# Optimization experiments

Measured on AMD Instinct MI355X. Metric: run time of the kernel, lower is better.

The kernel has to match this reference:

```python
import jax, jax.numpy as jnp
import numpy as np

D = 256   # model dim
M = 64    # num mechanisms
B = 4
S = 8192


def setup_inputs() -> dict:
    key = jax.random.key(0)
    ks = jax.random.split(key, 16)
    n = jax.random.normal
    inp = {
        "x": n(ks[0], (B, S, D), jnp.float32),
        "context": n(ks[1], (B, S, D), jnp.float32),
        # stacked per-mechanism params (m, out, in) etc.
        "Wm": n(ks[2], (M, D, D), jnp.float32) * (1.0 / np.sqrt(D)),
        "bm": n(ks[3], (M, D), jnp.float32) * 0.02,
        "cm": n(ks[4], (M, D), jnp.float32),           # characteristics (1,1,dim) per node
        "um": n(ks[5], (M, D), jnp.float32) * (1.0 / np.sqrt(D)),  # timing_gate weight
        "vm": n(ks[6], (M,), jnp.float32) * 0.02,       # timing_gate bias
        # selector: Linear(d, 2d) -> GELU -> Linear(2d, m)
        "W1": n(ks[7], (2 * D, D), jnp.float32) * (1.0 / np.sqrt(D)),
        "b1": n(ks[8], (2 * D,), jnp.float32) * 0.02,
        "W2": n(ks[9], (M, 2 * D), jnp.float32) * (1.0 / np.sqrt(2 * D)),
        "b2": n(ks[10], (M,), jnp.float32) * 0.02,
        # integrate: Linear(2d, d)
        "Wi": n(ks[11], (D, 2 * D), jnp.float32) * (1.0 / np.sqrt(2 * D)),
        "bi": n(ks[12], (D,), jnp.float32) * 0.02,
    }
    return inp


def reference(x, context, Wm, bm, cm, um, vm, W1, b1, W2, b2, Wi, bi):
    # selector: softmax over mechanisms (b, s, m)
    h = jax.nn.gelu(jnp.einsum('bsd,ed->bse', context, W1) + b1, approximate=False)
    scores = jax.nn.softmax(jnp.einsum('bse,me->bsm', h, W2) + b2, axis=-1)

    # per-mechanism sigmoid timing gate (b, s, m)
    gate = jax.nn.sigmoid(jnp.einsum('bsd,md->bsm', x, um) + vm)

    # combined weight a[b,s,m] = softmax_score * gate; then
    # selected = sum_m a * (x @ Wm.T + bm + cm)  -- contracted without
    # materializing the (b, s, m, d) stack the torch loop builds.
    a = scores * gate                               # (b, s, m)
    selected = jnp.einsum('bsm,bse,mde->bsd', a, x, Wm) \
             + jnp.einsum('bsm,md->bsd', a, bm + cm)

    # integrate(concat([x, selected]))
    cat = jnp.concatenate([x, selected], axis=-1)   # (b, s, 2d)
    integrated = jnp.einsum('bse,de->bsd', cat, Wi) + bi
    return integrated
```

## Files before the change

kernel.cpp:

```cpp
#include <hip/hip_runtime.h>
#include <cstdint>
#include <cstddef>


typedef _Float16 f16;
typedef f16 f16x8 __attribute__((ext_vector_type(8)));
typedef float f32x4 __attribute__((ext_vector_type(4)));
typedef float f32x16 __attribute__((ext_vector_type(16)));

#define DEV __device__ __forceinline__

DEV uint32_t swz128(uint32_t b) { return b ^ (((b >> 7) & 7u) << 4); }

DEV void gload_lds16(const void* g, void* l) {
  __builtin_amdgcn_global_load_lds(
      (const __attribute__((address_space(1))) unsigned int*)g,
      (__attribute__((address_space(3))) unsigned int*)l, 16, 0, 0);
}

DEV f16x8 cvt8(float4 u0, float4 u1) {
  f16x8 v = {(f16)u0.x, (f16)u0.y, (f16)u0.z, (f16)u0.w,
             (f16)u1.x, (f16)u1.y, (f16)u1.z, (f16)u1.w};
  return v;
}

__global__ void prep_b_kernel(const float* __restrict__ S, f16* __restrict__ dst,
                              int K, int BN, int total) {
  int t = blockIdx.x * 256 + threadIdx.x;
  if (t >= total) return;
  int gpc = BN * 8;
  int g = t % gpc;
  int c = (t / gpc) % (K / 64);
  int cb = t / (gpc * (K / 64));
  int ks = g / (BN * 4);
  int rem = g % (BN * 4);
  int col = rem >> 2;
  int kg = rem & 3;
  int J = cb * BN + col;
  int k = c * 64 + ks * 32 + kg * 8;
  const float* s = S + (size_t)J * K + k;
  float4 u0 = *(const float4*)s;
  float4 u1 = *(const float4*)(s + 4);
  f16* chunk = dst + (size_t)(cb * (K / 64) + c) * (BN * 64);
  *(f16x8*)((char*)chunk + swz128((uint32_t)g * 16)) = cvt8(u0, u1);
}

__global__ void prep_wcat_kernel(const float* __restrict__ Wm,
                                 const float* __restrict__ bm,
                                 const float* __restrict__ cm,
                                 f16* __restrict__ dst) {
  int t = blockIdx.x * 256 + threadIdx.x;
  if (t >= 4 * 257 * 512) return;
  int g = t & 511;
  int gc = t >> 9;
  int c = gc % 257;
  int cb = gc / 257;
  int kstep = g >> 7;
  int khalf = (g >> 6) & 1;
  int col = cb * 64 + (g & 63);
  int k0 = kstep * 16 + khalf * 8;
  f16x8 v;
  if (c < 256) {
    int m = c & 63;
    int e0 = (c >> 6) * 64 + k0;
    const float* s = Wm + ((size_t)m * 256 + col) * 256 + e0;
    float4 u0 = *(const float4*)s;
    float4 u1 = *(const float4*)(s + 4);
    v = cvt8(u0, u1);
  } else {
#pragma unroll
    for (int j = 0; j < 8; ++j) {
      int k = k0 + j;
      v[j] = (f16)(bm[k * 256 + col] + cm[k * 256 + col]);
    }
  }
  *(f16x8*)(dst + ((size_t)(cb * 260 + c)) * 4096 + (size_t)g * 8) = v;
}

template <int BN, int NCHUNK, int A0C, int EPI>
__global__ __launch_bounds__(BN == 256 ? 512 : 256, 2)
void gemm_tpl(const float* __restrict__ A0, int lda0,
              const f16* __restrict__ A1, int lda1,
              const f16* __restrict__ Bt,
              const float* __restrict__ bias,
              float* __restrict__ outF, f16* __restrict__ outH, int ldo) {
  constexpr int WAVES = (BN == 256) ? 8 : 4;
  constexpr int THREADS = WAVES * 64;
  constexpr int WC = (BN == 256) ? 4 : 1;
  constexpr int WR = WAVES / WC;
  constexpr int RT = 128 / (WR * 16);
  constexpr int CT = (BN / WC) / 16;

  __shared__ alignas(16) f16 sA[2][128 * 64];
  __shared__ alignas(16) f16 sB[2][BN * 64];

  const int tid = threadIdx.x;
  const int lane = tid & 63;
  const int wid = tid >> 6;
  const int wr = wid / WC, wc = wid % WC;
  const int rb = blockIdx.x, cb = blockIdx.y;

  auto stageB = [&](int c, int buf) {
    const char* src = (const char*)(Bt + (size_t)(cb * NCHUNK + c) * (BN * 64));
#pragma unroll
    for (int it = 0; it < (BN * 64 * 2) / (THREADS * 16); ++it) {
      int off = (it * THREADS + tid) * 16;
      gload_lds16(src + off, (char*)&sB[buf][0] + off);
    }
  };
  auto stageA = [&](int c, int buf) {
#pragma unroll
    for (int it = 0; it < 1024 / THREADS; ++it) {
      int gg = it * THREADS + tid;
      int row = gg >> 3, eg = gg & 7;
      size_t rowG = (size_t)rb * 128 + row;
      f16x8 v;
      if (A0C > 0 && c < A0C) {
        const float* s = A0 + rowG * lda0 + c * 64 + eg * 8;
        float4 u0 = *(const float4*)s;
        float4 u1 = *(const float4*)(s + 4);
        v = cvt8(u0, u1);
      } else {
        v = *(const f16x8*)(A1 + rowG * lda1 + (c - A0C) * 64 + eg * 8);
      }
      *(f16x8*)((char*)&sA[buf][0] + swz128((uint32_t)(row * 128 + eg * 16))) = v;
    }
  };

  f32x4 acc[RT][CT];
#pragma unroll
  for (int i = 0; i < RT; ++i)
#pragma unroll
    for (int j = 0; j < CT; ++j) acc[i][j] = (f32x4){0.f, 0.f, 0.f, 0.f};

  stageB(0, 0);
  stageA(0, 0);
  __syncthreads();

  for (int c = 0; c < NCHUNK; ++c) {
    int cur = c & 1;
    if (c + 1 < NCHUNK) {
      stageB(c + 1, cur ^ 1);
      stageA(c + 1, cur ^ 1);
    }
#pragma unroll
    for (int ks = 0; ks < 2; ++ks) {
      f16x8 af[RT], bf[CT];
#pragma unroll
      for (int rt = 0; rt < RT; ++rt) {
        int row = wr * (RT * 16) + rt * 16 + (lane & 15);
        af[rt] = *(const f16x8*)((const char*)&sA[cur][0] +
                                 swz128((uint32_t)(row * 128 + ks * 64 + (lane >> 4) * 16)));
      }
#pragma unroll
      for (int ct = 0; ct < CT; ++ct) {
        int col = wc * (CT * 16) + ct * 16 + (lane & 15);
        bf[ct] = *(const f16x8*)((const char*)&sB[cur][0] +
                                 swz128((uint32_t)(((ks * BN + col) * 4 + (lane >> 4)) * 16)));
      }
#pragma unroll
      for (int rt = 0; rt < RT; ++rt)
#pragma unroll
        for (int ct = 0; ct < CT; ++ct)
          acc[rt][ct] = __builtin_amdgcn_mfma_f32_16x16x32_f16(af[rt], bf[ct], acc[rt][ct], 0, 0, 0);
    }
    __syncthreads();
  }

#pragma unroll
  for (int rt = 0; rt < RT; ++rt)
#pragma unroll
    for (int ct = 0; ct < CT; ++ct)
#pragma unroll
      for (int i = 0; i < 4; ++i) {
        size_t row = (size_t)rb * 128 + wr * (RT * 16) + rt * 16 + (lane >> 4) * 4 + i;
        int colG = cb * BN + wc * (CT * 16) + ct * 16 + (lane & 15);
        float v = acc[rt][ct][i];
        if constexpr (EPI == 0) {
          if (bias) v += bias[colG];
          outF[row * ldo + colG] = v;
        } else {
          v += bias[colG];
          float ge = 0.5f * v * (1.0f + erff(v * 0.70710678118f));
          outH[row * ldo + colG] = (f16)ge;
        }
      }
}

__global__ void selector_finish(const float* __restrict__ logits,
                                const float* __restrict__ glog,
                                const float* __restrict__ b2,
                                const float* __restrict__ vm,
                                f16* __restrict__ a16s) {
  int n = blockIdx.x * 4 + (threadIdx.x >> 6);
  int m = threadIdx.x & 63;
  float l = logits[(size_t)n * 64 + m] + b2[m];
  float mx = l;
#pragma unroll
  for (int o = 32; o; o >>= 1) mx = fmaxf(mx, __shfl_xor(mx, o));
  float p = expf(l - mx);
  float s = p;
#pragma unroll
  for (int o = 32; o; o >>= 1) s += __shfl_xor(s, o);
  float g = glog[(size_t)n * 64 + m] + vm[m];
  float gate = 1.0f / (1.0f + expf(-g));
  int rb = n >> 8, row = n & 255, gg = m >> 3, j = m & 7;
  a16s[(size_t)rb * 16384 + gg * 2048 + row * 8 + j] = (f16)(p / s * gate);
}

__global__ __launch_bounds__(256, 2)
void big_gemm(const float* __restrict__ x, const f16* __restrict__ a16s,
              const f16* __restrict__ Wcat, f16* __restrict__ sel) {
  __shared__ alignas(16) f16 sAa[8 * 256 * 8];

  const int tid = threadIdx.x;
  const int lane = tid & 63;
  const int wid = tid >> 6;
  const int l31 = lane & 31;
  const int khalf = lane >> 5;
  const int bid = blockIdx.x;
  const int xcd = bid & 7;
  const int cb = xcd >> 1;
  const int rb = (xcd & 1) * 64 + (bid >> 3);
  const char* Wb = (const char*)(Wcat + (size_t)cb * 260 * 4096);
  const int rbase = wid * 64 + l31;

  {
    const char* aSrc = (const char*)(a16s + (size_t)rb * 16384);
#pragma unroll
    for (int it = 0; it < 8; ++it) {
      int off = (it * 256 + tid) * 16;
      gload_lds16(aSrc + off, (char*)sAa + off);
    }
  }
  asm volatile("s_waitcnt vmcnt(0)" ::: "memory");
  __builtin_amdgcn_s_barrier();

  const int bOff = khalf * 1024 + l31 * 16;

  f32x16 acc[2][2];
#pragma unroll
  for (int i = 0; i < 2; ++i)
#pragma unroll
    for (int j = 0; j < 2; ++j)
#pragma unroll
      for (int r = 0; r < 16; ++r) acc[i][j][r] = 0.f;

  f16x8 xv[2][4];
  auto loadXV = [&](int er) {
#pragma unroll
    for (int rt = 0; rt < 2; ++rt)
#pragma unroll
      for (int ks = 0; ks < 4; ++ks) {
        const float* s = x + ((size_t)rb * 256 + rbase + rt * 32) * 256
                           + er * 64 + ks * 16 + khalf * 8;
        float4 u0 = *(const float4*)s;
        float4 u1 = *(const float4*)(s + 4);
        xv[rt][ks] = cvt8(u0, u1);
      }
  };
  loadXV(0);

  f16x8 bf0[8], bf1[8];
#pragma unroll
  for (int ks = 0; ks < 4; ++ks)
#pragma unroll
    for (int ct = 0; ct < 2; ++ct) {
      bf0[ks * 2 + ct] = *(const f16x8*)(Wb + 0 * 8192 + bOff + ks * 2048 + ct * 512);
      bf1[ks * 2 + ct] = *(const f16x8*)(Wb + 1 * 8192 + bOff + ks * 2048 + ct * 512);
    }

  for (int q8g = 0; q8g < 32; ++q8g) {
    const int q8 = q8g * 8;
    if ((q8 & 63) == 0 && q8 > 0) loadXV(q8 >> 6);
    f16x8 as_cur[2];
    {
      int g = (q8 & 63) >> 3;
#pragma unroll
      for (int rt = 0; rt < 2; ++rt)
        as_cur[rt] = *(const f16x8*)((const char*)sAa + ((g * 256) + rbase + rt * 32) * 16);
    }
#pragma unroll
    for (int u = 0; u < 8; ++u) {
      const int q = q8 + u;
      f16x8 af[2][4];
#pragma unroll
      for (int rt = 0; rt < 2; ++rt)
#pragma unroll
        for (int ks = 0; ks < 4; ++ks)
          af[rt][ks] = xv[rt][ks] * as_cur[rt][u];
      const char* nsrc = Wb + (size_t)(q + 2) * 8192 + bOff;
      if ((u & 1) == 0) {
        __builtin_amdgcn_s_setprio(1);
#pragma unroll
        for (int ks = 0; ks < 4; ++ks)
#pragma unroll
          for (int rt = 0; rt < 2; ++rt)
#pragma unroll
            for (int ct = 0; ct < 2; ++ct)
              acc[rt][ct] = __builtin_amdgcn_mfma_f32_32x32x16_f16(
                  af[rt][ks], bf0[ks * 2 + ct], acc[rt][ct], 0, 0, 0);
        __builtin_amdgcn_s_setprio(0);
#pragma unroll
        for (int ks = 0; ks < 4; ++ks)
#pragma unroll
          for (int ct = 0; ct < 2; ++ct)
            bf0[ks * 2 + ct] = *(const f16x8*)(nsrc + ks * 2048 + ct * 512);
      } else {
        __builtin_amdgcn_s_setprio(1);
#pragma unroll
        for (int ks = 0; ks < 4; ++ks)
#pragma unroll
          for (int rt = 0; rt < 2; ++rt)
#pragma unroll
            for (int ct = 0; ct < 2; ++ct)
              acc[rt][ct] = __builtin_amdgcn_mfma_f32_32x32x16_f16(
                  af[rt][ks], bf1[ks * 2 + ct], acc[rt][ct], 0, 0, 0);
        __builtin_amdgcn_s_setprio(0);
#pragma unroll
        for (int ks = 0; ks < 4; ++ks)
#pragma unroll
          for (int ct = 0; ct < 2; ++ct)
            bf1[ks * 2 + ct] = *(const f16x8*)(nsrc + ks * 2048 + ct * 512);
      }
    }
  }

#pragma unroll
  for (int ks = 0; ks < 4; ++ks)
#pragma unroll
    for (int rt = 0; rt < 2; ++rt) {
      int g = ks * 2 + khalf;
      f16x8 af = *(const f16x8*)((const char*)sAa + ((g * 256) + rbase + rt * 32) * 16);
#pragma unroll
      for (int ct = 0; ct < 2; ++ct)
        acc[rt][ct] = __builtin_amdgcn_mfma_f32_32x32x16_f16(
            af, bf0[ks * 2 + ct], acc[rt][ct], 0, 0, 0);
    }

#pragma unroll
  for (int rt = 0; rt < 2; ++rt)
#pragma unroll
    for (int ct = 0; ct < 2; ++ct)
#pragma unroll
      for (int r = 0; r < 16; ++r) {
        int rowin = (r & 3) + 8 * (r >> 2) + 4 * khalf;
        size_t row = (size_t)rb * 256 + wid * 64 + rt * 32 + rowin;
        int col = cb * 64 + ct * 32 + l31;
        sel[row * 256 + col] = (f16)acc[rt][ct][r];
      }
}

extern "C" void kernel_launch(void* const* d_in, const int* in_sizes, int n_in,
                              void* d_out, int out_size, void* d_ws, size_t ws_size,
                              hipStream_t stream) {
  (void)in_sizes; (void)n_in; (void)out_size;
  const float* x   = (const float*)d_in[0];
  const float* ctx = (const float*)d_in[1];
  const float* Wm  = (const float*)d_in[2];
  const float* bm  = (const float*)d_in[3];
  const float* cm  = (const float*)d_in[4];
  const float* um  = (const float*)d_in[5];
  const float* vm  = (const float*)d_in[6];
  const float* W1  = (const float*)d_in[7];
  const float* b1  = (const float*)d_in[8];
  const float* W2  = (const float*)d_in[9];
  const float* b2  = (const float*)d_in[10];
  const float* Wi  = (const float*)d_in[11];
  const float* bi  = (const float*)d_in[12];
  float* out = (float*)d_out;

  char* ws = (char*)d_ws;
  size_t off = 0;
  f16* Wcat = (f16*)(ws + off); off += (size_t)4 * 260 * 4096 * 2;
  f16* W1t  = (f16*)(ws + off); off += (size_t)512 * 256 * 2;
  f16* W2t  = (f16*)(ws + off); off += (size_t)64 * 512 * 2;
  f16* umt  = (f16*)(ws + off); off += (size_t)64 * 256 * 2;
  f16* Wit  = (f16*)(ws + off); off += (size_t)256 * 512 * 2;
  f16* h16  = (f16*)(ws + off); off += (size_t)32768 * 512 * 2;
  float* logits = (float*)(ws + off); off += (size_t)32768 * 64 * 4;
  float* glog   = (float*)(ws + off); off += (size_t)32768 * 64 * 4;
  f16* a16s  = (f16*)(ws + off); off += (size_t)32768 * 64 * 2;
  f16* sel16 = (f16*)(ws + off); off += (size_t)32768 * 256 * 2;
  if (ws_size < off) return;

  prep_wcat_kernel<<<dim3(2056), dim3(256), 0, stream>>>(Wm, bm, cm, Wcat);
  prep_b_kernel<<<dim3(16384 / 256), dim3(256), 0, stream>>>(W1, W1t, 256, 256, 16384);
  prep_b_kernel<<<dim3(4096 / 256),  dim3(256), 0, stream>>>(W2, W2t, 512, 64, 4096);
  prep_b_kernel<<<dim3(2048 / 256),  dim3(256), 0, stream>>>(um, umt, 256, 64, 2048);
  prep_b_kernel<<<dim3(16384 / 256), dim3(256), 0, stream>>>(Wi, Wit, 512, 256, 16384);

  gemm_tpl<256, 4, 4, 1><<<dim3(256, 2), dim3(512), 0, stream>>>(
      ctx, 256, nullptr, 0, W1t, b1, nullptr, h16, 512);
  gemm_tpl<64, 4, 4, 0><<<dim3(256, 1), dim3(256), 0, stream>>>(
      x, 256, nullptr, 0, umt, nullptr, glog, nullptr, 64);
  gemm_tpl<64, 8, 0, 0><<<dim3(256, 1), dim3(256), 0, stream>>>(
      nullptr, 0, h16, 512, W2t, nullptr, logits, nullptr, 64);
  selector_finish<<<dim3(32768 / 4), dim3(256), 0, stream>>>(logits, glog, b2, vm, a16s);

  big_gemm<<<dim3(512), dim3(256), 0, stream>>>(x, a16s, Wcat, sel16);

  gemm_tpl<256, 8, 4, 0><<<dim3(256, 1), dim3(512), 0, stream>>>(
      x, 256, sel16, 256, Wit, bi, out, nullptr, 256);
}
```

Measured before the change: 376.2 us.

## Stage Wcat chunks through LDS ring buffer with 8 waves per block

The big_gemm kernel now uses 512 threads (8 waves split 4 rows by 2 columns) instead of 4 waves each covering both column tiles. Weight chunks are prefetched into a 4-slot LDS ring via global_load_lds rather than loaded per-wave into registers straight from global memory. The aim is to cut redundant global B loads across waves and free registers for more occupancy. The cost is two block-wide barriers per mechanism-chunk step, plus each wave now recomputing the x*a scaling for half as many MFMAs.

```diff
diff --git a/kernel.cpp b/kernel.cpp
--- a/kernel.cpp
+++ b/kernel.cpp
@@ -208,14 +208,17 @@
   a16s[(size_t)rb * 16384 + gg * 2048 + row * 8 + j] = (f16)(p / s * gate);
 }
 
-__global__ __launch_bounds__(256, 2)
+__global__ __launch_bounds__(512, 4)
 void big_gemm(const float* __restrict__ x, const f16* __restrict__ a16s,
               const f16* __restrict__ Wcat, f16* __restrict__ sel) {
+  __shared__ alignas(16) f16 sB[4][64 * 64];
   __shared__ alignas(16) f16 sAa[8 * 256 * 8];
 
   const int tid = threadIdx.x;
   const int lane = tid & 63;
   const int wid = tid >> 6;
+  const int wr = wid >> 1;
+  const int wc = wid & 1;
   const int l31 = lane & 31;
   const int khalf = lane >> 5;
   const int bid = blockIdx.x;
@@ -223,28 +226,32 @@
   const int cb = xcd >> 1;
   const int rb = (xcd & 1) * 64 + (bid >> 3);
   const char* Wb = (const char*)(Wcat + (size_t)cb * 260 * 4096);
-  const int rbase = wid * 64 + l31;
+  const int rbase = wr * 64 + l31;
+
+  char* const sBb = (char*)&sB[0][0];
+
+  auto stageChunk = [&](int c, int slotIdx) {
+    gload_lds16(Wb + (size_t)c * 8192 + tid * 16, sBb + slotIdx * 8192 + tid * 16);
+  };
 
   {
     const char* aSrc = (const char*)(a16s + (size_t)rb * 16384);
 #pragma unroll
-    for (int it = 0; it < 8; ++it) {
-      int off = (it * 256 + tid) * 16;
+    for (int it = 0; it < 4; ++it) {
+      int off = (it * 512 + tid) * 16;
       gload_lds16(aSrc + off, (char*)sAa + off);
     }
   }
+  stageChunk(0, 0);
+  stageChunk(1, 1);
   asm volatile("s_waitcnt vmcnt(0)" ::: "memory");
   __builtin_amdgcn_s_barrier();
 
-  const int bOff = khalf * 1024 + l31 * 16;
-
-  f32x16 acc[2][2];
-#pragma unroll
-  for (int i = 0; i < 2; ++i)
-#pragma unroll
-    for (int j = 0; j < 2; ++j)
-#pragma unroll
-      for (int r = 0; r < 16; ++r) acc[i][j][r] = 0.f;
+  f32x16 acc[2];
+#pragma unroll
+  for (int rt = 0; rt < 2; ++rt)
+#pragma unroll
+    for (int r = 0; r < 16; ++r) acc[rt][r] = 0.f;
 
   f16x8 xv[2][4];
   auto loadXV = [&](int er) {
@@ -259,96 +266,74 @@
         xv[rt][ks] = cvt8(u0, u1);
       }
   };
-  loadXV(0);
-
-  f16x8 bf0[8], bf1[8];
-#pragma unroll
-  for (int ks = 0; ks < 4; ++ks)
-#pragma unroll
-    for (int ct = 0; ct < 2; ++ct) {
-      bf0[ks * 2 + ct] = *(const f16x8*)(Wb + 0 * 8192 + bOff + ks * 2048 + ct * 512);
-      bf1[ks * 2 + ct] = *(const f16x8*)(Wb + 1 * 8192 + bOff + ks * 2048 + ct * 512);
-    }
+
+  const int bOff = khalf * 1024 + wc * 512 + l31 * 16;
+
+  f16x8 as8[2];
 
   for (int q8g = 0; q8g < 32; ++q8g) {
     const int q8 = q8g * 8;
-    if ((q8 & 63) == 0 && q8 > 0) loadXV(q8 >> 6);
-    f16x8 as_cur[2];
-    {
-      int g = (q8 & 63) >> 3;
-#pragma unroll
-      for (int rt = 0; rt < 2; ++rt)
-        as_cur[rt] = *(const f16x8*)((const char*)sAa + ((g * 256) + rbase + rt * 32) * 16);
-    }
 #pragma unroll
     for (int u = 0; u < 8; ++u) {
       const int q = q8 + u;
-      f16x8 af[2][4];
-#pragma unroll
-      for (int rt = 0; rt < 2; ++rt)
-#pragma unroll
-        for (int ks = 0; ks < 4; ++ks)
-          af[rt][ks] = xv[rt][ks] * as_cur[rt][u];
-      const char* nsrc = Wb + (size_t)(q + 2) * 8192 + bOff;
-      if ((u & 1) == 0) {
-        __builtin_amdgcn_s_setprio(1);
-#pragma unroll
-        for (int ks = 0; ks < 4; ++ks)
-#pragma unroll
-          for (int rt = 0; rt < 2; ++rt)
-#pragma unroll
-            for (int ct = 0; ct < 2; ++ct)
-              acc[rt][ct] = __builtin_amdgcn_mfma_f32_32x32x16_f16(
-                  af[rt][ks], bf0[ks * 2 + ct], acc[rt][ct], 0, 0, 0);
-        __builtin_amdgcn_s_setprio(0);
-#pragma unroll
-        for (int ks = 0; ks < 4; ++ks)
-#pragma unroll
-          for (int ct = 0; ct < 2; ++ct)
-            bf0[ks * 2 + ct] = *(const f16x8*)(nsrc + ks * 2048 + ct * 512);
-      } else {
-        __builtin_amdgcn_s_setprio(1);
-#pragma unroll
-        for (int ks = 0; ks < 4; ++ks)
-#pragma unroll
-          for (int rt = 0; rt < 2; ++rt)
-#pragma unroll
-            for (int ct = 0; ct < 2; ++ct)
-              acc[rt][ct] = __builtin_amdgcn_mfma_f32_32x32x16_f16(
-                  af[rt][ks], bf1[ks * 2 + ct], acc[rt][ct], 0, 0, 0);
-        __builtin_amdgcn_s_setprio(0);
-#pragma unroll
-        for (int ks = 0; ks < 4; ++ks)
-#pragma unroll
-          for (int ct = 0; ct < 2; ++ct)
-            bf1[ks * 2 + ct] = *(const f16x8*)(nsrc + ks * 2048 + ct * 512);
-      }
-    }
-  }
-
-#pragma unroll
-  for (int ks = 0; ks < 4; ++ks)
-#pragma unroll
-    for (int rt = 0; rt < 2; ++rt) {
-      int g = ks * 2 + khalf;
-      f16x8 af = *(const f16x8*)((const char*)sAa + ((g * 256) + rbase + rt * 32) * 16);
-#pragma unroll
-      for (int ct = 0; ct < 2; ++ct)
-        acc[rt][ct] = __builtin_amdgcn_mfma_f32_32x32x16_f16(
-            af, bf0[ks * 2 + ct], acc[rt][ct], 0, 0, 0);
-    }
+      if (u == 0) {
+        if ((q8 & 63) == 0) loadXV(q8 >> 6);
+        int g = (q8 & 63) >> 3;
+#pragma unroll
+        for (int rt = 0; rt < 2; ++rt)
+          as8[rt] = *(const f16x8*)((const char*)sAa + ((g * 256) + rbase + rt * 32) * 16);
+      }
+      const char* slotB = sBb + (size_t)((q8g * 8 + u) & 3) * 8192 + bOff;
+      f16x8 bf[4];
+#pragma unroll
+      for (int ks = 0; ks < 4; ++ks)
+        bf[ks] = *(const f16x8*)(slotB + ks * 2048);
+      stageChunk(q + 2, (u + 2) & 3);
+      asm volatile("s_waitcnt vmcnt(1)" ::: "memory");
+      __builtin_amdgcn_s_barrier();
+      asm volatile("s_waitcnt lgkmcnt(0)" ::: "memory");
+      __builtin_amdgcn_sched_barrier(0);
+      __builtin_amdgcn_s_setprio(1);
+#pragma unroll
+      for (int ks = 0; ks < 4; ++ks)
+#pragma unroll
+        for (int rt = 0; rt < 2; ++rt) {
+          f16x8 af = xv[rt][ks] * as8[rt][u];
+          acc[rt] = __builtin_amdgcn_mfma_f32_32x32x16_f16(af, bf[ks], acc[rt], 0, 0, 0);
+        }
+      __builtin_amdgcn_s_setprio(0);
+      __builtin_amdgcn_sched_barrier(0);
+      __builtin_amdgcn_s_barrier();
+    }
+  }
+
+  {
+    const char* slotB = sBb + 0 * 8192 + bOff;
+    f16x8 bf[4];
+#pragma unroll
+    for (int ks = 0; ks < 4; ++ks)
+      bf[ks] = *(const f16x8*)(slotB + ks * 2048);
+    asm volatile("s_waitcnt lgkmcnt(0)" ::: "memory");
+    __builtin_amdgcn_sched_barrier(0);
+#pragma unroll
+    for (int ks = 0; ks < 4; ++ks)
+#pragma unroll
+      for (int rt = 0; rt < 2; ++rt) {
+        int g = ks * 2 + khalf;
+        f16x8 af = *(const f16x8*)((const char*)sAa + ((g * 256) + rbase + rt * 32) * 16);
+        acc[rt] = __builtin_amdgcn_mfma_f32_32x32x16_f16(af, bf[ks], acc[rt], 0, 0, 0);
+      }
+  }
 
 #pragma unroll
   for (int rt = 0; rt < 2; ++rt)
 #pragma unroll
-    for (int ct = 0; ct < 2; ++ct)
-#pragma unroll
-      for (int r = 0; r < 16; ++r) {
-        int rowin = (r & 3) + 8 * (r >> 2) + 4 * khalf;
-        size_t row = (size_t)rb * 256 + wid * 64 + rt * 32 + rowin;
-        int col = cb * 64 + ct * 32 + l31;
-        sel[row * 256 + col] = (f16)acc[rt][ct][r];
-      }
+    for (int r = 0; r < 16; ++r) {
+      int rowin = (r & 3) + 8 * (r >> 2) + 4 * khalf;
+      size_t row = (size_t)rb * 256 + wr * 64 + rt * 32 + rowin;
+      int col = cb * 64 + wc * 32 + l31;
+      sel[row * 256 + col] = (f16)acc[rt][r];
+    }
 }
 
 extern "C" void kernel_launch(void* const* d_in, const int* in_sizes, int n_in,
@@ -398,7 +383,7 @@
       nullptr, 0, h16, 512, W2t, nullptr, logits, nullptr, 64);
   selector_finish<<<dim3(32768 / 4), dim3(256), 0, stream>>>(logits, glog, b2, vm, a16s);
 
-  big_gemm<<<dim3(512), dim3(256), 0, stream>>>(x, a16s, Wcat, sel16);
+  big_gemm<<<dim3(512), dim3(512), 0, stream>>>(x, a16s, Wcat, sel16);
 
   gemm_tpl<256, 8, 4, 0><<<dim3(256, 1), dim3(512), 0, stream>>>(
       x, 256, sel16, 256, Wit, bi, out, nullptr, 256);
```

After: 363.4 us. 3.4% less time.
